# Kernel optimization log

Measured on AMD Instinct MI355X. Metric: run time of the kernel, lower is better.

The kernel has to match this reference:

```python
import jax, jax.numpy as jnp
import numpy as np

N = 50000      # nodes
E = 800000     # edges (before self loops)
D_IN = 64      # input atom feature dim
HID = 128      # hidden_dim
HEADS = 4
C = HID // HEADS  # 32 per-head channels
ED = 12        # edge feature dim
L = 4          # num GAT layers
EPS = 1e-5


def setup_inputs() -> dict:
    key = jax.random.key(0)
    ks = jax.random.split(key, 10)
    s = 0.1
    return {
        "x": jax.random.normal(ks[0], (N, D_IN), jnp.float32),
        "edge_index": jax.random.randint(ks[1], (2, E), 0, N, dtype=jnp.int32),
        "edge_attr": jax.random.uniform(ks[2], (E, ED), jnp.float32),
        "Wp": jax.random.normal(ks[3], (D_IN, HID), jnp.float32) * s,
        "bp": jnp.zeros((HID,), jnp.float32),
        "W": jax.random.normal(ks[4], (L, HID, HID), jnp.float32) * s,
        "We": jax.random.normal(ks[5], (L, ED, HID), jnp.float32) * s,
        "att_src": jax.random.normal(ks[6], (L, HEADS, C), jnp.float32) * s,
        "att_dst": jax.random.normal(ks[7], (L, HEADS, C), jnp.float32) * s,
        "att_edge": jax.random.normal(ks[8], (L, HEADS, C), jnp.float32) * s,
        "bias": jnp.zeros((L, HID), jnp.float32),
        "gamma": jnp.ones((L, HID), jnp.float32),
        "beta": jnp.zeros((L, HID), jnp.float32),
    }


def _gat_layer(h, src, dst, ea_full, W, We, a_s, a_d, a_e, b):
    # PyG GATConv: x' = x W -> [N, heads, C]; attention uses edge features, msg = alpha * x'_src
    xp = (h @ W).reshape(N, HEADS, C)
    e_emb = (ea_full @ We).reshape(-1, HEADS, C)          # [E', heads, C]
    a_src = (xp * a_s).sum(-1)                            # [N, heads]
    a_dst = (xp * a_d).sum(-1)
    a = a_src[src] + a_dst[dst] + (e_emb * a_e).sum(-1)   # [E', heads]
    a = jax.nn.leaky_relu(a, 0.2)
    # segment softmax over destination node neighborhoods
    amax = jax.ops.segment_max(a, dst, num_segments=N)
    ex = jnp.exp(a - amax[dst])
    denom = jax.ops.segment_sum(ex, dst, num_segments=N)
    alpha = ex / denom[dst]                               # [E', heads]
    msg = alpha[:, :, None] * xp[src]                     # [E', heads, C]
    out = jax.ops.segment_sum(msg, dst, num_segments=N)   # [N, heads, C]
    return out.reshape(N, HID) + b


def reference(x, edge_index, edge_attr, Wp, bp, W, We, att_src, att_dst, att_edge, bias, gamma, beta):
    # PyG GATConv add_self_loops=True with fill_value='mean' for edge_attr
    loop = jnp.arange(N, dtype=edge_index.dtype)
    src = jnp.concatenate([edge_index[0], loop])
    dst = jnp.concatenate([edge_index[1], loop])
    ea_mean = edge_attr.mean(0)
    ea_full = jnp.concatenate([edge_attr, jnp.broadcast_to(ea_mean, (N, ED))], 0)

    h = jax.nn.relu(x @ Wp + bp)
    for i in range(L):
        h_in = h
        h = _gat_layer(h, src, dst, ea_full, W[i], We[i], att_src[i], att_dst[i], att_edge[i], bias[i])
        # BatchNorm1d (training-mode batch statistics)
        mu = h.mean(0)
        var = ((h - mu) ** 2).mean(0)
        h = gamma[i] * (h - mu) / jnp.sqrt(var + EPS) + beta[i]
        h = jax.nn.relu(h)
        if i > 0:
            h = h + h_in
    return h
```

## Files before the change

### kernel.cpp

```cpp
#include <hip/hip_runtime.h>

constexpr int N_NODES = 50000;
constexpr int N_EDGES = 800000;
constexpr int N_ETOT  = N_EDGES + N_NODES;
constexpr int HID     = 128;
constexpr int HEADS   = 4;
constexpr int ED      = 12;
constexpr int LAYERS  = 4;
constexpr float BN_EPS = 1e-5f;
constexpr int EB = (N_ETOT + 255) / 256;
constexpr int GB = (N_NODES + 63) / 64;
constexpr int WB = (LAYERS * HID * HID + 255) / 256;
constexpr int CHUNK  = 2048;
constexpr int NCHUNK = (N_ETOT + CHUNK - 1) / CHUNK;
constexpr int NB     = (N_NODES + 127) / 128;
constexpr int F_TOT  = NB * NCHUNK;
constexpr int SB3    = (F_TOT + 255) / 256;

typedef __attribute__((ext_vector_type(8))) short short8;
typedef __attribute__((ext_vector_type(4))) float floatx4;

__device__ inline unsigned bf16pair(float a, float b) {
    unsigned ua = __float_as_uint(a), ub = __float_as_uint(b);
    ua = (ua + 0x7FFFu + ((ua >> 16) & 1u)) >> 16;
    ub = (ub + 0x7FFFu + ((ub >> 16) & 1u)) >> 16;
    return ua | (ub << 16);
}

__launch_bounds__(256)
__global__ void pre1_kernel(const int* __restrict__ dst, int* __restrict__ counts,
                            const float* __restrict__ ea, float* __restrict__ easum,
                            const float* __restrict__ W, unsigned short* __restrict__ wb,
                            const float* __restrict__ A, const float* __restrict__ B,
                            const float* __restrict__ bias, float* __restrict__ C,
                            unsigned* __restrict__ Cb) {
    __shared__ float smem[64 * 128];
    int bid = blockIdx.x, t = threadIdx.x;
    if (bid < GB) {
        constexpr int K = 64;
        const float4* B4 = (const float4*)B;
        float4* Bs4 = (float4*)smem;
#pragma unroll
        for (int i = t; i < K * 32; i += 256) Bs4[i] = B4[i];
        __syncthreads();

        int c0 = (t & 15) * 8;
        int r0 = (t >> 4) * 4;
        int rbase = bid * 64 + r0;

        float acc[4][8];
#pragma unroll
        for (int j = 0; j < 4; j++)
#pragma unroll
            for (int c = 0; c < 8; c++) acc[j][c] = 0.f;

        const float4* A4 = (const float4*)A;
        int rg[4];
#pragma unroll
        for (int j = 0; j < 4; j++) rg[j] = min(rbase + j, N_NODES - 1);

        for (int kk = 0; kk < K; kk += 4) {
            float4 av[4];
#pragma unroll
            for (int j = 0; j < 4; j++) av[j] = A4[(size_t)rg[j] * (K / 4) + (kk >> 2)];
            float a_arr[4][4];
#pragma unroll
            for (int j = 0; j < 4; j++) {
                a_arr[j][0] = av[j].x; a_arr[j][1] = av[j].y;
                a_arr[j][2] = av[j].z; a_arr[j][3] = av[j].w;
            }
#pragma unroll
            for (int jj = 0; jj < 4; jj++) {
                float4 b0 = Bs4[(kk + jj) * 32 + (c0 >> 2)];
                float4 b1 = Bs4[(kk + jj) * 32 + (c0 >> 2) + 1];
#pragma unroll
                for (int j = 0; j < 4; j++) {
                    float a = a_arr[j][jj];
                    acc[j][0] += a * b0.x; acc[j][1] += a * b0.y;
                    acc[j][2] += a * b0.z; acc[j][3] += a * b0.w;
                    acc[j][4] += a * b1.x; acc[j][5] += a * b1.y;
                    acc[j][6] += a * b1.z; acc[j][7] += a * b1.w;
                }
            }
        }

#pragma unroll
        for (int j = 0; j < 4; j++) {
            int r = rbase + j;
            if (r < N_NODES) {
                float o[8];
#pragma unroll
                for (int c = 0; c < 8; c++) o[c] = fmaxf(acc[j][c] + bias[c0 + c], 0.f);
                ((float4*)(C + (size_t)r * 128 + c0))[0] = make_float4(o[0], o[1], o[2], o[3]);
                ((float4*)(C + (size_t)r * 128 + c0 + 4))[0] = make_float4(o[4], o[5], o[6], o[7]);
                uint4 pk;
                pk.x = bf16pair(o[0], o[1]); pk.y = bf16pair(o[2], o[3]);
                pk.z = bf16pair(o[4], o[5]); pk.w = bf16pair(o[6], o[7]);
                ((uint4*)(Cb + (size_t)r * 64 + (c0 >> 1)))[0] = pk;
            }
        }
    } else if (bid < GB + NCHUNK) {
        int chunk = bid - GB;
        int* lh = (int*)smem;
        for (int i = t; i < NB; i += 256) lh[i] = 0;
        __syncthreads();
        int e0 = chunk * CHUNK;
        int eend = min(e0 + CHUNK, N_ETOT);
        for (int e = e0 + t; e < eend; e += 256) {
            int d = (e < N_EDGES) ? dst[e] : (e - N_EDGES);
            atomicAdd(&lh[d >> 7], 1);
        }
        __syncthreads();
        for (int i = t; i < NB; i += 256) counts[(size_t)chunk * NB + i] = lh[i];
    } else if (bid < GB + NCHUNK + 256) {
        int b2 = bid - GB - NCHUNK;
        float* ls = smem;
        if (t < 12) ls[t] = 0.f;
        __syncthreads();
        float loc[12];
#pragma unroll
        for (int d = 0; d < 12; d++) loc[d] = 0.f;
        for (int e = b2 * 256 + t; e < N_EDGES; e += 256 * 256) {
            const float* er = ea + (size_t)e * ED;
#pragma unroll
            for (int d = 0; d < 12; d++) loc[d] += er[d];
        }
#pragma unroll
        for (int d = 0; d < 12; d++) atomicAdd(&ls[d], loc[d]);
        __syncthreads();
        if (t < 12) atomicAdd(&easum[t], ls[t]);
    } else {
        int idx = (bid - GB - NCHUNK - 256) * 256 + t;
        if (idx < LAYERS * HID * HID) {
            int l = idx >> 14;
            int k = (idx >> 7) & 127;
            int n = idx & 127;
            unsigned u = __float_as_uint(W[idx]);
            u = (u + 0x7FFFu + ((u >> 16) & 1u)) >> 16;
            int kt = k >> 5, q = (k & 31) >> 3, j = k & 7;
            int nt = n >> 4, c = n & 15;
            int lane = q * 16 + c;
            wb[(size_t)l * 16384 + ((size_t)(kt * 8 + nt) * 64 + lane) * 8 + j] =
                (unsigned short)u;
        }
    }
}

__global__ void blocksum2_kernel(const int* __restrict__ counts, int* __restrict__ bsum) {
    __shared__ int sd[256];
    int t = threadIdx.x;
    int j = blockIdx.x * 256 + t;
    int v = 0;
    if (j < F_TOT) {
        int bb = j / NCHUNK, cc = j - bb * NCHUNK;
        v = counts[(size_t)cc * NB + bb];
    }
    sd[t] = v;
    __syncthreads();
#pragma unroll
    for (int off = 128; off; off >>= 1) {
        if (t < off) sd[t] += sd[t + off];
        __syncthreads();
    }
    if (t == 0) bsum[blockIdx.x] = sd[0];
}

__launch_bounds__(256)
__global__ void pre2_kernel(const int* __restrict__ bsum, int* __restrict__ boff,
                            int* __restrict__ chunkbase, int* __restrict__ rowp,
                            const float* __restrict__ easum,
                            const float* __restrict__ We, const float* __restrict__ att_edge,
                            float* __restrict__ wea_all, float* __restrict__ aloop) {
    int t = threadIdx.x;
    if (blockIdx.x == 0) {
        __shared__ int sd[256];
        int b = 3 * t;
        int v0 = (b + 0 < SB3) ? bsum[b + 0] : 0;
        int v1 = (b + 1 < SB3) ? bsum[b + 1] : 0;
        int v2 = (b + 2 < SB3) ? bsum[b + 2] : 0;
        int tot = v0 + v1 + v2;
        sd[t] = tot;
        __syncthreads();
#pragma unroll
        for (int off = 1; off < 256; off <<= 1) {
            int u = (t >= off) ? sd[t - off] : 0;
            __syncthreads();
            sd[t] += u;
            __syncthreads();
        }
        int excl = sd[t] - tot;
        if (b + 0 < SB3) boff[b + 0] = excl;
        if (b + 1 < SB3) boff[b + 1] = excl + v0;
        if (b + 2 < SB3) boff[b + 2] = excl + v0 + v1;
        if (t == 255) {
            chunkbase[F_TOT] = sd[255];
            rowp[N_NODES] = N_ETOT;
        }
    } else {
        __shared__ float em[12];
        __shared__ float weash[LAYERS * ED * HEADS];
        if (t < 12) em[t] = easum[t] / (float)N_EDGES;
        if (t < LAYERS * ED * HEADS) {
            int l = t / (ED * HEADS);
            int r = t % (ED * HEADS);
            int d = r / HEADS;
            int h = r % HEADS;
            float sum = 0.f;
#pragma unroll
            for (int c = 0; c < 32; c++)
                sum += We[((size_t)(l * ED + d)) * HID + h * 32 + c] *
                       att_edge[(l * HEADS + h) * 32 + c];
            wea_all[t] = sum;
            weash[t] = sum;
        }
        __syncthreads();
        if (t < LAYERS * HEADS) {
            int l = t / HEADS, h = t % HEADS;
            float s = 0.f;
#pragma unroll
            for (int d = 0; d < 12; d++) s += em[d] * weash[l * ED * HEADS + d * HEADS + h];
            aloop[t] = s;
        }
    }
}

__global__ void addback_kernel(const int* __restrict__ counts, const int* __restrict__ boff,
                               int* __restrict__ chunkbase) {
    __shared__ int sd[256];
    int t = threadIdx.x;
    int j = blockIdx.x * 256 + t;
    int v = 0;
    if (j < F_TOT) {
        int bb = j / NCHUNK, cc = j - bb * NCHUNK;
        v = counts[(size_t)cc * NB + bb];
    }
    sd[t] = v;
    __syncthreads();
#pragma unroll
    for (int off = 1; off < 256; off <<= 1) {
        int u = (t >= off) ? sd[t - off] : 0;
        __syncthreads();
        sd[t] += u;
        __syncthreads();
    }
    if (j < F_TOT) chunkbase[j] = sd[t] - v + boff[blockIdx.x];
}

__launch_bounds__(256)
__global__ void pre3_kernel(const unsigned short* __restrict__ hAb,
                            const unsigned short* __restrict__ wb,
                            const float* __restrict__ att_s, const float* __restrict__ att_d,
                            unsigned* __restrict__ xpb,
                            float* __restrict__ asrc, float* __restrict__ adst,
                            const int* __restrict__ src, const int* __restrict__ dst,
                            const int* __restrict__ chunkbase, int2* __restrict__ bucketed) {
    __shared__ float smem[4 * 16 * 129];
    int t = threadIdx.x;
    if (blockIdx.x >= GB) {
        int chunk = blockIdx.x - GB;
        int* lb = (int*)smem;
        int* lh = lb + NB;
        for (int i = t; i < NB; i += 256) {
            lb[i] = chunkbase[(size_t)i * NCHUNK + chunk];
            lh[i] = 0;
        }
        __syncthreads();
        int e0 = chunk * CHUNK;
        int eend = min(e0 + CHUNK, N_ETOT);
        for (int e = e0 + t; e < eend; e += 256) {
            int s, d;
            if (e < N_EDGES) { s = src[e]; d = dst[e]; }
            else             { s = d = e - N_EDGES; }
            int b = d >> 7;
            int lr = atomicAdd(&lh[b], 1);
            bucketed[lb[b] + lr] = make_int2(s, e | ((d & 127) << 20));
        }
        return;
    }
    int bid = blockIdx.x;
    float (*lds)[16][129] = (float (*)[16][129])smem;
    int w = t >> 6, lane = t & 63;
    int rbase = bid * 64 + w * 16;
    int mrow = lane & 15, quad = lane >> 4;

    floatx4 acc[8];
#pragma unroll
    for (int nt = 0; nt < 8; nt++) acc[nt] = (floatx4){0.f, 0.f, 0.f, 0.f};

    int arow = min(rbase + mrow, N_NODES - 1);
    const short8* wb8 = (const short8*)wb;
#pragma unroll
    for (int kt = 0; kt < 4; kt++) {
        short8 afrag = *(const short8*)(hAb + (size_t)arow * 128 + kt * 32 + quad * 8);
#pragma unroll
        for (int nt = 0; nt < 8; nt++) {
            short8 bfrag = wb8[(kt * 8 + nt) * 64 + lane];
            acc[nt] = __builtin_amdgcn_mfma_f32_16x16x32_bf16(afrag, bfrag, acc[nt], 0, 0, 0);
        }
    }
#pragma unroll
    for (int nt = 0; nt < 8; nt++)
#pragma unroll
        for (int rr = 0; rr < 4; rr++)
            lds[w][quad * 4 + rr][nt * 16 + mrow] = acc[nt][rr];

    int row = lane >> 2, h = lane & 3;
    int r = rbase + row;
    float vals[32];
    float ps = 0.f, pd = 0.f;
#pragma unroll
    for (int c = 0; c < 32; c++) {
        float v = lds[w][row][h * 32 + c];
        vals[c] = v;
        ps += v * att_s[h * 32 + c];
        pd += v * att_d[h * 32 + c];
    }
    if (r < N_NODES) {
        unsigned* dstp = xpb + (size_t)r * 64 + h * 16;
#pragma unroll
        for (int qq = 0; qq < 4; qq++) {
            uint4 o;
            o.x = bf16pair(vals[qq * 8 + 0], vals[qq * 8 + 1]);
            o.y = bf16pair(vals[qq * 8 + 2], vals[qq * 8 + 3]);
            o.z = bf16pair(vals[qq * 8 + 4], vals[qq * 8 + 5]);
            o.w = bf16pair(vals[qq * 8 + 6], vals[qq * 8 + 7]);
            ((uint4*)dstp)[qq] = o;
        }
        asrc[r * 4 + h] = ps;
        adst[r * 4 + h] = pd;
    }
}

__launch_bounds__(256)
__global__ void csrd_kernel(const int2* __restrict__ bucketed, const int* __restrict__ chunkbase,
                            int2* __restrict__ csr, int* __restrict__ rowp) {
    __shared__ int hist[128], exc[128], cur[128];
    int b = blockIdx.x, t = threadIdx.x;
    int base = chunkbase[(size_t)b * NCHUNK];
    int cend = chunkbase[(size_t)(b + 1) * NCHUNK];
    int cnt = cend - base;
    if (t < 128) { hist[t] = 0; cur[t] = 0; }
    __syncthreads();
    for (int i = t; i < cnt; i += 256)
        atomicAdd(&hist[(bucketed[base + i].y >> 20) & 127], 1);
    __syncthreads();
    if (t < 128) exc[t] = hist[t];
    __syncthreads();
#pragma unroll
    for (int off = 1; off < 128; off <<= 1) {
        int u = (t < 128 && t >= off) ? exc[t - off] : 0;
        __syncthreads();
        if (t < 128) exc[t] += u;
        __syncthreads();
    }
    if (t < 128) {
        exc[t] -= hist[t];
        int node = b * 128 + t;
        if (node < N_NODES) rowp[node] = base + exc[t];
    }
    __syncthreads();
    for (int i = t; i < cnt; i += 256) {
        int2 r = bucketed[base + i];
        int dl = (r.y >> 20) & 127;
        int lr = atomicAdd(&cur[dl], 1);
        csr[base + exc[dl] + lr] = make_int2(r.x, r.y & 0xFFFFF);
    }
}

__launch_bounds__(256)
__global__ void pre4_kernel(const int2* __restrict__ csr, const float* __restrict__ ea,
                            const float* __restrict__ wea_all, const float* __restrict__ aloop,
                            uint2* __restrict__ aecsr) {
    __shared__ float wsh[LAYERS * ED * HEADS];
    __shared__ float lsh[LAYERS * HEADS];
    int t = threadIdx.x;
    if (t < LAYERS * ED * HEADS) wsh[t] = wea_all[t];
    if (t < LAYERS * HEADS) lsh[t] = aloop[t];
    __syncthreads();
    int i = blockIdx.x * 256 + t;
    if (i >= N_ETOT) return;
    int e = csr[i].y;
    float a[LAYERS][4];
    if (e < N_EDGES) {
        float er[12];
        const float* ep = ea + (size_t)e * ED;
#pragma unroll
        for (int d = 0; d < 12; d++) er[d] = ep[d];
#pragma unroll
        for (int l = 0; l < LAYERS; l++)
#pragma unroll
            for (int h = 0; h < 4; h++) {
                float s = 0.f;
#pragma unroll
                for (int d = 0; d < 12; d++) s += er[d] * wsh[l * 48 + d * 4 + h];
                a[l][h] = s;
            }
    } else {
#pragma unroll
        for (int l = 0; l < LAYERS; l++)
#pragma unroll
            for (int h = 0; h < 4; h++) a[l][h] = lsh[l * 4 + h];
    }
#pragma unroll
    for (int l = 0; l < LAYERS; l++)
        aecsr[(size_t)l * N_ETOT + i] =
            make_uint2(bf16pair(a[l][0], a[l][1]), bf16pair(a[l][2], a[l][3]));
}

template <int ADD>
__launch_bounds__(256)
__global__ void gemm_fused_kernel(const float* __restrict__ outb,
                                  const float* __restrict__ bnsum,
                                  const float* __restrict__ bnsum2,
                                  const float* __restrict__ gamma,
                                  const float* __restrict__ beta,
                                  float* __restrict__ hA,
                                  const unsigned short* __restrict__ wb,
                                  const float* __restrict__ att_s,
                                  const float* __restrict__ att_d,
                                  unsigned* __restrict__ xpb,
                                  float* __restrict__ asrc, float* __restrict__ adst) {
    __shared__ float lds[4][16][129];
    __shared__ float sc_s[128], sh_s[128];
    int t = threadIdx.x;
    if (t < 128) {
        float mu = bnsum[t] / (float)N_NODES;
        float var = bnsum2[t] / (float)N_NODES - mu * mu;
        float inv = rsqrtf(var + BN_EPS);
        float g = gamma[t] * inv;
        sc_s[t] = g;
        sh_s[t] = beta[t] - mu * g;
    }
    __syncthreads();

    int w = t >> 6, lane = t & 63;
    int rbase = blockIdx.x * 64 + w * 16;
    int mrow = lane & 15, quad = lane >> 4;
    int arow = rbase + mrow;
    bool owner = arow < N_NODES;
    int ar = min(arow, N_NODES - 1);

    floatx4 acc[8];
#pragma unroll
    for (int nt = 0; nt < 8; nt++) acc[nt] = (floatx4){0.f, 0.f, 0.f, 0.f};

    const short8* wb8 = (const short8*)wb;
#pragma unroll
    for (int kt = 0; kt < 4; kt++) {
        int cb = kt * 32 + quad * 8;
        const float4* ob = (const float4*)(outb + (size_t)ar * 128 + cb);
        float4 o0 = ob[0], o1 = ob[1];
        float v[8];
        v[0] = fmaxf(o0.x * sc_s[cb + 0] + sh_s[cb + 0], 0.f);
        v[1] = fmaxf(o0.y * sc_s[cb + 1] + sh_s[cb + 1], 0.f);
        v[2] = fmaxf(o0.z * sc_s[cb + 2] + sh_s[cb + 2], 0.f);
        v[3] = fmaxf(o0.w * sc_s[cb + 3] + sh_s[cb + 3], 0.f);
        v[4] = fmaxf(o1.x * sc_s[cb + 4] + sh_s[cb + 4], 0.f);
        v[5] = fmaxf(o1.y * sc_s[cb + 5] + sh_s[cb + 5], 0.f);
        v[6] = fmaxf(o1.z * sc_s[cb + 6] + sh_s[cb + 6], 0.f);
        v[7] = fmaxf(o1.w * sc_s[cb + 7] + sh_s[cb + 7], 0.f);
        if (ADD) {
            const float4* hp = (const float4*)(hA + (size_t)ar * 128 + cb);
            float4 h0 = hp[0], h1 = hp[1];
            v[0] += h0.x; v[1] += h0.y; v[2] += h0.z; v[3] += h0.w;
            v[4] += h1.x; v[5] += h1.y; v[6] += h1.z; v[7] += h1.w;
        }
        if (owner) {
            float4* hw = (float4*)(hA + (size_t)ar * 128 + cb);
            hw[0] = make_float4(v[0], v[1], v[2], v[3]);
            hw[1] = make_float4(v[4], v[5], v[6], v[7]);
        }
        uint4 pk;
        pk.x = bf16pair(v[0], v[1]); pk.y = bf16pair(v[2], v[3]);
        pk.z = bf16pair(v[4], v[5]); pk.w = bf16pair(v[6], v[7]);
        short8 afrag = *(short8*)&pk;
#pragma unroll
        for (int nt = 0; nt < 8; nt++) {
            short8 bfrag = wb8[(kt * 8 + nt) * 64 + lane];
            acc[nt] = __builtin_amdgcn_mfma_f32_16x16x32_bf16(afrag, bfrag, acc[nt], 0, 0, 0);
        }
    }

#pragma unroll
    for (int nt = 0; nt < 8; nt++)
#pragma unroll
        for (int rr = 0; rr < 4; rr++)
            lds[w][quad * 4 + rr][nt * 16 + mrow] = acc[nt][rr];

    int row = lane >> 2, h = lane & 3;
    int r = rbase + row;
    float vals[32];
    float ps = 0.f, pd = 0.f;
#pragma unroll
    for (int c = 0; c < 32; c++) {
        float v = lds[w][row][h * 32 + c];
        vals[c] = v;
        ps += v * att_s[h * 32 + c];
        pd += v * att_d[h * 32 + c];
    }
    if (r < N_NODES) {
        unsigned* dstp = xpb + (size_t)r * 64 + h * 16;
#pragma unroll
        for (int qq = 0; qq < 4; qq++) {
            uint4 o;
            o.x = bf16pair(vals[qq * 8 + 0], vals[qq * 8 + 1]);
            o.y = bf16pair(vals[qq * 8 + 2], vals[qq * 8 + 3]);
            o.z = bf16pair(vals[qq * 8 + 4], vals[qq * 8 + 5]);
            o.w = bf16pair(vals[qq * 8 + 6], vals[qq * 8 + 7]);
            ((uint4*)dstp)[qq] = o;
        }
        asrc[r * 4 + h] = ps;
        adst[r * 4 + h] = pd;
    }
}

__launch_bounds__(256)
__global__ void node_kernel(const uint2* __restrict__ aecsr, const float* __restrict__ asrc,
                            const float* __restrict__ adst, const int* __restrict__ rowp,
                            const int2* __restrict__ csr, const unsigned* __restrict__ xpb,
                            float* __restrict__ out) {
    int gw = (blockIdx.x * blockDim.x + threadIdx.x) >> 6;
    int lane = threadIdx.x & 63;
    if (gw >= N_NODES) return;
    int sub = lane >> 4;
    int sl  = lane & 15;
    int h   = sl >> 2;
    int beg = rowp[gw], end = rowp[gw + 1];
    const uint4* xp4 = (const uint4*)xpb;
    float adh = adst[gw * 4 + h];

    float a[8];
#pragma unroll
    for (int c = 0; c < 8; c++) a[c] = 0.f;
    float den = 0.f;

#define PROC(JJ)                                                                 \
    {                                                                            \
        int2 se = csr[JJ];                                                       \
        uint2 ae = aecsr[JJ];                                                    \
        unsigned aw = (h & 2) ? ae.y : ae.x;                                     \
        float aeh = __uint_as_float((h & 1) ? (aw & 0xFFFF0000u) : (aw << 16));  \
        float ash = asrc[se.x * 4 + h];                                          \
        uint4 v = xp4[(size_t)se.x * 16 + sl];                                   \
        float lg = ash + adh + aeh;                                              \
        lg = (lg > 0.f) ? lg : 0.2f * lg;                                        \
        float ex = __expf(fminf(lg, 60.f));                                      \
        a[0] += ex * __uint_as_float(v.x << 16);                                 \
        a[1] += ex * __uint_as_float(v.x & 0xFFFF0000u);                         \
        a[2] += ex * __uint_as_float(v.y << 16);                                 \
        a[3] += ex * __uint_as_float(v.y & 0xFFFF0000u);                         \
        a[4] += ex * __uint_as_float(v.z << 16);                                 \
        a[5] += ex * __uint_as_float(v.z & 0xFFFF0000u);                         \
        a[6] += ex * __uint_as_float(v.w << 16);                                 \
        a[7] += ex * __uint_as_float(v.w & 0xFFFF0000u);                         \
        den += ex;                                                               \
    }

    int j = beg + sub;
    for (; j + 12 < end; j += 16) {
        PROC(j); PROC(j + 4); PROC(j + 8); PROC(j + 12);
    }
    for (; j < end; j += 4) PROC(j);
#undef PROC

#pragma unroll
    for (int c = 0; c < 8; c++) {
        a[c] += __shfl_xor(a[c], 16);
        a[c] += __shfl_xor(a[c], 32);
    }
    den += __shfl_xor(den, 16);
    den += __shfl_xor(den, 32);
    float inv = 1.0f / den;
    if (sub == 0) {
        float* op = out + (size_t)gw * 128 + sl * 8;
        ((float4*)op)[0] = make_float4(a[0] * inv, a[1] * inv, a[2] * inv, a[3] * inv);
        ((float4*)op)[1] = make_float4(a[4] * inv, a[5] * inv, a[6] * inv, a[7] * inv);
    }
}

__launch_bounds__(256)
__global__ void bnstats_kernel(const float* __restrict__ h, float* __restrict__ bnsum,
                               float* __restrict__ bnsum2) {
    __shared__ float ls[256], ls2[256];
    int t = threadIdx.x;
    int c = t & 127, half = t >> 7;
    int r0 = blockIdx.x * 128;
    float s = 0.f, s2 = 0.f;
    int rend = min(r0 + 128, N_NODES);
    for (int r = r0 + half; r < rend; r += 2) {
        float v = h[(size_t)r * 128 + c];
        s += v; s2 += v * v;
    }
    ls[t] = s; ls2[t] = s2;
    __syncthreads();
    if (half == 0) {
        s += ls[t + 128]; s2 += ls2[t + 128];
        atomicAdd(&bnsum[c], s);
        atomicAdd(&bnsum2[c], s2);
    }
}

__launch_bounds__(256)
__global__ void finalupd_kernel(const float* __restrict__ outb, const float* __restrict__ bnsum,
                                const float* __restrict__ bnsum2, const float* __restrict__ gamma,
                                const float* __restrict__ beta, const float* __restrict__ hA,
                                float* __restrict__ dst) {
    __shared__ float sc_s[128], sh_s[128];
    int t = threadIdx.x;
    if (t < 128) {
        float mu = bnsum[t] / (float)N_NODES;
        float var = bnsum2[t] / (float)N_NODES - mu * mu;
        float inv = rsqrtf(var + BN_EPS);
        float g = gamma[t] * inv;
        sc_s[t] = g;
        sh_s[t] = beta[t] - mu * g;
    }
    __syncthreads();
    int i = blockIdx.x * blockDim.x + t;
    if (i >= N_NODES * 32) return;
    int c4 = (i & 31) * 4;
    float4 o = ((const float4*)outb)[i];
    float4 hh = ((const float4*)hA)[i];
    float4 v;
    v.x = fmaxf(o.x * sc_s[c4 + 0] + sh_s[c4 + 0], 0.f) + hh.x;
    v.y = fmaxf(o.y * sc_s[c4 + 1] + sh_s[c4 + 1], 0.f) + hh.y;
    v.z = fmaxf(o.z * sc_s[c4 + 2] + sh_s[c4 + 2], 0.f) + hh.z;
    v.w = fmaxf(o.w * sc_s[c4 + 3] + sh_s[c4 + 3], 0.f) + hh.w;
    ((float4*)dst)[i] = v;
}

extern "C" void kernel_launch(void* const* d_in, const int* in_sizes, int n_in,
                              void* d_out, int out_size, void* d_ws, size_t ws_size,
                              hipStream_t stream) {
    const float* x          = (const float*)d_in[0];
    const int*   edge_index = (const int*)d_in[1];
    const float* edge_attr  = (const float*)d_in[2];
    const float* Wp         = (const float*)d_in[3];
    const float* bp         = (const float*)d_in[4];
    const float* W          = (const float*)d_in[5];
    const float* We         = (const float*)d_in[6];
    const float* att_src    = (const float*)d_in[7];
    const float* att_dst    = (const float*)d_in[8];
    const float* att_edge   = (const float*)d_in[9];
    const float* gamma      = (const float*)d_in[11];
    const float* beta       = (const float*)d_in[12];
    float* outp = (float*)d_out;

    const int* ei_src = edge_index;
    const int* ei_dst = edge_index + N_EDGES;

    char* p = (char*)d_ws;
    auto alloc = [&](size_t nbytes) {
        char* r = p;
        p += (nbytes + 255) & ~(size_t)255;
        return r;
    };
    float* easum    = (float*)alloc(16 * 4);
    float* bnsumall = (float*)alloc((size_t)LAYERS * 256 * 4);
    size_t zero_bytes = (char*)(bnsumall + LAYERS * 256) - (char*)easum;

    float* hA       = (float*)alloc((size_t)N_NODES * 128 * 4);
    unsigned* hAb   = (unsigned*)alloc((size_t)N_NODES * 64 * 4);
    unsigned* xpb   = (unsigned*)alloc((size_t)N_NODES * 64 * 4);
    float* outb     = (float*)alloc((size_t)N_NODES * 128 * 4);
    float* asrc     = (float*)alloc((size_t)N_NODES * 4 * 4);
    float* adst     = (float*)alloc((size_t)N_NODES * 4 * 4);
    float* wea_all  = (float*)alloc((LAYERS * 48 + 16) * 4);
    float* aloop    = wea_all + LAYERS * 48;
    unsigned short* wb = (unsigned short*)alloc((size_t)LAYERS * 16384 * 2);
    int* rowp       = (int*)alloc(((size_t)N_NODES + 1) * 4);
    int* counts     = (int*)alloc((size_t)F_TOT * 4);
    int* chunkbase  = (int*)alloc(((size_t)F_TOT + 1) * 4);
    int2* bucketed  = (int2*)alloc((size_t)N_ETOT * 8);
    int2* csr       = (int2*)alloc((size_t)N_ETOT * 8);
    uint2* aecsr    = (uint2*)alloc((size_t)LAYERS * N_ETOT * 8);
    int* bsum       = (int*)alloc(1024 * 4);
    int* boff       = (int*)alloc(1024 * 4);

    (void)hipMemsetAsync(easum, 0, zero_bytes, stream);

    pre1_kernel<<<GB + NCHUNK + 256 + WB, 256, 0, stream>>>(
        ei_dst, counts, edge_attr, easum, W, wb, x, Wp, bp, hA, hAb);
    blocksum2_kernel<<<SB3, 256, 0, stream>>>(counts, bsum);
    pre2_kernel<<<2, 256, 0, stream>>>(bsum, boff, chunkbase, rowp, easum, We, att_edge,
                                       wea_all, aloop);
    addback_kernel<<<SB3, 256, 0, stream>>>(counts, boff, chunkbase);
    pre3_kernel<<<GB + NCHUNK, 256, 0, stream>>>(
        (const unsigned short*)hAb, wb, att_src, att_dst, xpb, asrc, adst,
        ei_src, ei_dst, chunkbase, bucketed);
    csrd_kernel<<<NB, 256, 0, stream>>>(bucketed, chunkbase, csr, rowp);
    pre4_kernel<<<EB, 256, 0, stream>>>(csr, edge_attr, wea_all, aloop, aecsr);

    for (int l = 0; l < LAYERS; l++) {
        float* bnsum  = bnsumall + l * 256;
        float* bnsum2 = bnsum + 128;
        node_kernel<<<(N_NODES + 3) / 4, 256, 0, stream>>>(
            aecsr + (size_t)l * N_ETOT, asrc, adst, rowp, csr, xpb, outb);
        bnstats_kernel<<<(N_NODES + 127) / 128, 256, 0, stream>>>(outb, bnsum, bnsum2);
        if (l < LAYERS - 1) {
            if (l == 0)
                gemm_fused_kernel<0><<<GB, 256, 0, stream>>>(
                    outb, bnsum, bnsum2, gamma + l * 128, beta + l * 128, hA,
                    wb + (size_t)(l + 1) * 16384, att_src + (l + 1) * 128,
                    att_dst + (l + 1) * 128, xpb, asrc, adst);
            else
                gemm_fused_kernel<1><<<GB, 256, 0, stream>>>(
                    outb, bnsum, bnsum2, gamma + l * 128, beta + l * 128, hA,
                    wb + (size_t)(l + 1) * 16384, att_src + (l + 1) * 128,
                    att_dst + (l + 1) * 128, xpb, asrc, adst);
        } else {
            finalupd_kernel<<<(N_NODES * 32 + 255) / 256, 256, 0, stream>>>(
                outb, bnsum, bnsum2, gamma + l * 128, beta + l * 128, hA, outp);
        }
    }
}
```

Baseline: 569.5 us.

## Stage projection weights, sub-sort CSR by source block, widen node-kernel lanes

The input projection GEMM now loads its weight matrix into shared memory in two 32-row stages, halving the shared memory footprint so more blocks can reside per CU. The CSR build kernel now bins edges by destination and also by a coarse source-node block, so each node's neighbour list is grouped by source region, which should improve locality of the gathers. The node aggregation kernel has each lane cover 16 channels using two 16-byte loads, so each wave processes 8 edges at a time instead of 4, at the cost of more registers and an extra shuffle reduction step.

```diff
diff --git a/kernel.cpp b/kernel.cpp
--- a/kernel.cpp
+++ b/kernel.cpp
@@ -34,15 +34,11 @@
                             const float* __restrict__ A, const float* __restrict__ B,
                             const float* __restrict__ bias, float* __restrict__ C,
                             unsigned* __restrict__ Cb) {
-    __shared__ float smem[64 * 128];
+    __shared__ float smem[32 * 128];
     int bid = blockIdx.x, t = threadIdx.x;
     if (bid < GB) {
-        constexpr int K = 64;
         const float4* B4 = (const float4*)B;
         float4* Bs4 = (float4*)smem;
-#pragma unroll
-        for (int i = t; i < K * 32; i += 256) Bs4[i] = B4[i];
-        __syncthreads();
 
         int c0 = (t & 15) * 8;
         int r0 = (t >> 4) * 4;
@@ -59,27 +55,35 @@
 #pragma unroll
         for (int j = 0; j < 4; j++) rg[j] = min(rbase + j, N_NODES - 1);
 
-        for (int kk = 0; kk < K; kk += 4) {
-            float4 av[4];
-#pragma unroll
-            for (int j = 0; j < 4; j++) av[j] = A4[(size_t)rg[j] * (K / 4) + (kk >> 2)];
-            float a_arr[4][4];
-#pragma unroll
-            for (int j = 0; j < 4; j++) {
-                a_arr[j][0] = av[j].x; a_arr[j][1] = av[j].y;
-                a_arr[j][2] = av[j].z; a_arr[j][3] = av[j].w;
-            }
-#pragma unroll
-            for (int jj = 0; jj < 4; jj++) {
-                float4 b0 = Bs4[(kk + jj) * 32 + (c0 >> 2)];
-                float4 b1 = Bs4[(kk + jj) * 32 + (c0 >> 2) + 1];
+#pragma unroll
+        for (int stage = 0; stage < 2; stage++) {
+            if (stage) __syncthreads();
+#pragma unroll
+            for (int i = t; i < 32 * 32; i += 256) Bs4[i] = B4[stage * 1024 + i];
+            __syncthreads();
+            for (int kk = 0; kk < 32; kk += 4) {
+                float4 av[4];
+#pragma unroll
+                for (int j = 0; j < 4; j++)
+                    av[j] = A4[(size_t)rg[j] * 16 + stage * 8 + (kk >> 2)];
+                float a_arr[4][4];
 #pragma unroll
                 for (int j = 0; j < 4; j++) {
-                    float a = a_arr[j][jj];
-                    acc[j][0] += a * b0.x; acc[j][1] += a * b0.y;
-                    acc[j][2] += a * b0.z; acc[j][3] += a * b0.w;
-                    acc[j][4] += a * b1.x; acc[j][5] += a * b1.y;
-                    acc[j][6] += a * b1.z; acc[j][7] += a * b1.w;
+                    a_arr[j][0] = av[j].x; a_arr[j][1] = av[j].y;
+                    a_arr[j][2] = av[j].z; a_arr[j][3] = av[j].w;
+                }
+#pragma unroll
+                for (int jj = 0; jj < 4; jj++) {
+                    float4 b0 = Bs4[(kk + jj) * 32 + (c0 >> 2)];
+                    float4 b1 = Bs4[(kk + jj) * 32 + (c0 >> 2) + 1];
+#pragma unroll
+                    for (int j = 0; j < 4; j++) {
+                        float a = a_arr[j][jj];
+                        acc[j][0] += a * b0.x; acc[j][1] += a * b0.y;
+                        acc[j][2] += a * b0.z; acc[j][3] += a * b0.w;
+                        acc[j][4] += a * b1.x; acc[j][5] += a * b1.y;
+                        acc[j][6] += a * b1.z; acc[j][7] += a * b1.w;
+                    }
                 }
             }
         }
@@ -334,36 +338,49 @@
 __launch_bounds__(256)
 __global__ void csrd_kernel(const int2* __restrict__ bucketed, const int* __restrict__ chunkbase,
                             int2* __restrict__ csr, int* __restrict__ rowp) {
-    __shared__ int hist[128], exc[128], cur[128];
+    __shared__ int hist[2048], cur[2048], sd[256];
     int b = blockIdx.x, t = threadIdx.x;
     int base = chunkbase[(size_t)b * NCHUNK];
     int cend = chunkbase[(size_t)(b + 1) * NCHUNK];
     int cnt = cend - base;
-    if (t < 128) { hist[t] = 0; cur[t] = 0; }
-    __syncthreads();
-    for (int i = t; i < cnt; i += 256)
-        atomicAdd(&hist[(bucketed[base + i].y >> 20) & 127], 1);
-    __syncthreads();
-    if (t < 128) exc[t] = hist[t];
-    __syncthreads();
-#pragma unroll
-    for (int off = 1; off < 128; off <<= 1) {
-        int u = (t < 128 && t >= off) ? exc[t - off] : 0;
-        __syncthreads();
-        if (t < 128) exc[t] += u;
-        __syncthreads();
-    }
-    if (t < 128) {
-        exc[t] -= hist[t];
-        int node = b * 128 + t;
-        if (node < N_NODES) rowp[node] = base + exc[t];
-    }
+    for (int i = t; i < 2048; i += 256) hist[i] = 0;
     __syncthreads();
     for (int i = t; i < cnt; i += 256) {
         int2 r = bucketed[base + i];
-        int dl = (r.y >> 20) & 127;
-        int lr = atomicAdd(&cur[dl], 1);
-        csr[base + exc[dl] + lr] = make_int2(r.x, r.y & 0xFFFFF);
+        int bin = ((r.y >> 20) & 127) * 16 + (r.x >> 12);
+        atomicAdd(&hist[bin], 1);
+    }
+    __syncthreads();
+    int v[8];
+    int s = 0;
+#pragma unroll
+    for (int k = 0; k < 8; k++) { v[k] = hist[t * 8 + k]; s += v[k]; }
+    sd[t] = s;
+    __syncthreads();
+#pragma unroll
+    for (int off = 1; off < 256; off <<= 1) {
+        int u = (t >= off) ? sd[t - off] : 0;
+        __syncthreads();
+        sd[t] += u;
+        __syncthreads();
+    }
+    int running = sd[t] - s;
+#pragma unroll
+    for (int k = 0; k < 8; k++) {
+        hist[t * 8 + k] = running;
+        cur[t * 8 + k] = running;
+        running += v[k];
+    }
+    __syncthreads();
+    if (t < 128) {
+        int node = b * 128 + t;
+        if (node < N_NODES) rowp[node] = base + hist[t * 16];
+    }
+    for (int i = t; i < cnt; i += 256) {
+        int2 r = bucketed[base + i];
+        int bin = ((r.y >> 20) & 127) * 16 + (r.x >> 12);
+        int pos = base + atomicAdd(&cur[bin], 1);
+        csr[pos] = make_int2(r.x, r.y & 0xFFFFF);
     }
 }
 
@@ -522,16 +539,16 @@
     int gw = (blockIdx.x * blockDim.x + threadIdx.x) >> 6;
     int lane = threadIdx.x & 63;
     if (gw >= N_NODES) return;
-    int sub = lane >> 4;
-    int sl  = lane & 15;
-    int h   = sl >> 2;
+    int sub = lane >> 3;
+    int sl  = lane & 7;
+    int h   = sl >> 1;
     int beg = rowp[gw], end = rowp[gw + 1];
     const uint4* xp4 = (const uint4*)xpb;
     float adh = adst[gw * 4 + h];
 
-    float a[8];
-#pragma unroll
-    for (int c = 0; c < 8; c++) a[c] = 0.f;
+    float a[16];
+#pragma unroll
+    for (int c = 0; c < 16; c++) a[c] = 0.f;
     float den = 0.f;
 
 #define PROC(JJ)                                                                 \
@@ -541,40 +558,53 @@
         unsigned aw = (h & 2) ? ae.y : ae.x;                                     \
         float aeh = __uint_as_float((h & 1) ? (aw & 0xFFFF0000u) : (aw << 16));  \
         float ash = asrc[se.x * 4 + h];                                          \
-        uint4 v = xp4[(size_t)se.x * 16 + sl];                                   \
+        uint4 v0 = xp4[(size_t)se.x * 16 + sl * 2];                              \
+        uint4 v1 = xp4[(size_t)se.x * 16 + sl * 2 + 1];                          \
         float lg = ash + adh + aeh;                                              \
         lg = (lg > 0.f) ? lg : 0.2f * lg;                                        \
         float ex = __expf(fminf(lg, 60.f));                                      \
-        a[0] += ex * __uint_as_float(v.x << 16);                                 \
-        a[1] += ex * __uint_as_float(v.x & 0xFFFF0000u);                         \
-        a[2] += ex * __uint_as_float(v.y << 16);                                 \
-        a[3] += ex * __uint_as_float(v.y & 0xFFFF0000u);                         \
-        a[4] += ex * __uint_as_float(v.z << 16);                                 \
-        a[5] += ex * __uint_as_float(v.z & 0xFFFF0000u);                         \
-        a[6] += ex * __uint_as_float(v.w << 16);                                 \
-        a[7] += ex * __uint_as_float(v.w & 0xFFFF0000u);                         \
+        a[0]  += ex * __uint_as_float(v0.x << 16);                               \
+        a[1]  += ex * __uint_as_float(v0.x & 0xFFFF0000u);                       \
+        a[2]  += ex * __uint_as_float(v0.y << 16);                               \
+        a[3]  += ex * __uint_as_float(v0.y & 0xFFFF0000u);                       \
+        a[4]  += ex * __uint_as_float(v0.z << 16);                               \
+        a[5]  += ex * __uint_as_float(v0.z & 0xFFFF0000u);                       \
+        a[6]  += ex * __uint_as_float(v0.w << 16);                               \
+        a[7]  += ex * __uint_as_float(v0.w & 0xFFFF0000u);                       \
+        a[8]  += ex * __uint_as_float(v1.x << 16);                               \
+        a[9]  += ex * __uint_as_float(v1.x & 0xFFFF0000u);                       \
+        a[10] += ex * __uint_as_float(v1.y << 16);                               \
+        a[11] += ex * __uint_as_float(v1.y & 0xFFFF0000u);                       \
+        a[12] += ex * __uint_as_float(v1.z << 16);                               \
+        a[13] += ex * __uint_as_float(v1.z & 0xFFFF0000u);                       \
+        a[14] += ex * __uint_as_float(v1.w << 16);                               \
+        a[15] += ex * __uint_as_float(v1.w & 0xFFFF0000u);                       \
         den += ex;                                                               \
     }
 
     int j = beg + sub;
-    for (; j + 12 < end; j += 16) {
-        PROC(j); PROC(j + 4); PROC(j + 8); PROC(j + 12);
-    }
-    for (; j < end; j += 4) PROC(j);
+    for (; j + 8 < end; j += 16) {
+        PROC(j); PROC(j + 8);
+    }
+    for (; j < end; j += 8) PROC(j);
 #undef PROC
 
 #pragma unroll
-    for (int c = 0; c < 8; c++) {
+    for (int c = 0; c < 16; c++) {
+        a[c] += __shfl_xor(a[c], 8);
         a[c] += __shfl_xor(a[c], 16);
         a[c] += __shfl_xor(a[c], 32);
     }
+    den += __shfl_xor(den, 8);
     den += __shfl_xor(den, 16);
     den += __shfl_xor(den, 32);
     float inv = 1.0f / den;
     if (sub == 0) {
-        float* op = out + (size_t)gw * 128 + sl * 8;
+        float* op = out + (size_t)gw * 128 + sl * 16;
         ((float4*)op)[0] = make_float4(a[0] * inv, a[1] * inv, a[2] * inv, a[3] * inv);
         ((float4*)op)[1] = make_float4(a[4] * inv, a[5] * inv, a[6] * inv, a[7] * inv);
+        ((float4*)op)[2] = make_float4(a[8] * inv, a[9] * inv, a[10] * inv, a[11] * inv);
+        ((float4*)op)[3] = make_float4(a[12] * inv, a[13] * inv, a[14] * inv, a[15] * inv);
     }
 }
 
```

After: 803.8 us. 1.41x slower.
